# Optimization experiments

Measured on AMD Instinct MI355X. Metric: run time of the kernel, lower is better.

Reference implementation:

```python
import jax, jax.numpy as jnp
import numpy as np

N_EMBD = 512
N_HEAD = 8


def setup_inputs() -> dict:
    key = jax.random.key(0)
    k_x, k_aw, k_ab, k_pw, k_pb = jax.random.split(key, 5)
    B, T, E = 4, 2048, N_EMBD
    s = 1.0 / np.sqrt(E)
    return {
        "x": jax.random.normal(k_x, (B, T, E), dtype=jnp.float32),
        # torch Linear weight is [out, in]; store transposed for x @ W
        "c_attn_w": jax.random.uniform(k_aw, (E, 3 * E), jnp.float32, -s, s),
        "c_attn_b": jax.random.uniform(k_ab, (3 * E,), jnp.float32, -s, s),
        "c_proj_w": jax.random.uniform(k_pw, (E, E), jnp.float32, -s, s),
        "c_proj_b": jax.random.uniform(k_pb, (E,), jnp.float32, -s, s),
    }


def reference(x, c_attn_w, c_attn_b, c_proj_w, c_proj_b):
    B, T, E = x.shape
    H = N_HEAD
    D = E // H
    qkv = x @ c_attn_w + c_attn_b                      # [B,T,3E]
    q, k, v = jnp.split(qkv, 3, axis=2)
    # [B,T,E] -> [B,H,T,D]
    q = q.reshape(B, T, H, D).transpose(0, 2, 1, 3)
    k = k.reshape(B, T, H, D).transpose(0, 2, 1, 3)
    v = v.reshape(B, T, H, D).transpose(0, 2, 1, 3)
    scale = 1.0 / np.sqrt(D).astype(np.float32)
    scores = jnp.einsum("bhqd,bhkd->bhqk", q, k) * scale
    causal = jnp.tril(jnp.ones((T, T), dtype=bool))    # [T,T]
    scores = jnp.where(causal, scores, -jnp.inf)
    attn = jax.nn.softmax(scores, axis=-1)             # [B,H,T,T]
    y = jnp.einsum("bhqk,bhkd->bhqd", attn, v)         # [B,H,T,D]
    y = y.transpose(0, 2, 1, 3).reshape(B, T, E)
    return y @ c_proj_w + c_proj_b
```

## Files before the change

### kernel.cpp

```cpp
#include <hip/hip_runtime.h>
#include <math.h>

#define N_EMBD 512
#define N_HEAD 8
#define SEQ_T  2048
#define BATCH  4
#define QK_LD  1024

typedef __attribute__((ext_vector_type(8))) short bf16x8;
typedef __attribute__((ext_vector_type(4))) float f32x4;

#define CL 0.18033688f

#define WAITVM(N) asm volatile("s_waitcnt vmcnt(" #N ")" ::: "memory")

__device__ __forceinline__ unsigned short f2bf(float f) {
    union { float f; unsigned int u; } x; x.f = f;
    return (unsigned short)((x.u + 0x7FFFu + ((x.u >> 16) & 1u)) >> 16);
}
__device__ __forceinline__ unsigned pack_trunc(float a, float b) {
    union { float f; unsigned u; } x, y; x.f = a; y.f = b;
    return __builtin_amdgcn_perm(y.u, x.u, 0x07060302u);
}
__device__ __forceinline__ bf16x8 scale_frag(bf16x8 v, float c) {
    bf16x8 r;
    #pragma unroll
    for (int i = 0; i < 8; ++i) {
        union { unsigned u; float f; } x;
        x.u = ((unsigned)(unsigned short)v[i]) << 16;
        r[i] = (short)f2bf(x.f * c);
    }
    return r;
}

__device__ __forceinline__ void gl_lds16(const void* g, void* s) {
    __builtin_amdgcn_global_load_lds(
        (const __attribute__((address_space(1))) void*)g,
        (__attribute__((address_space(3))) void*)s, 16, 0, 0);
}

__global__ __launch_bounds__(256) void prep(
    const float* __restrict__ w1, unsigned short* __restrict__ w1t,
    const float* __restrict__ w2, unsigned short* __restrict__ w2t)
{
    __shared__ float t[32][33];
    const int bx = blockIdx.x, tid = threadIdx.x;
    const float* W; unsigned short* Wt; int N, tt, nb;
    if (bx < 768) { tt = bx;       W = w1; Wt = w1t; N = 1536; nb = 48; }
    else          { tt = bx - 768; W = w2; Wt = w2t; N = 512;  nb = 16; }
    const int n0 = (tt % nb) * 32, k0 = (tt / nb) * 32;
    const int tx = tid & 31, ty = tid >> 5;
    #pragma unroll
    for (int i = 0; i < 4; ++i)
        t[ty + i * 8][tx] = W[(size_t)(k0 + ty + i * 8) * N + n0 + tx];
    __syncthreads();
    #pragma unroll
    for (int i = 0; i < 4; ++i)
        Wt[(size_t)(n0 + ty + i * 8) * 512 + k0 + tx] = f2bf(t[tx][ty + i * 8]);
}

template <int BM, int BN, bool CVT_A, int OMODE>
__global__ __launch_bounds__(256) void gemm_mfma(
    const void* __restrict__ Asrc,
    const unsigned short* __restrict__ Bt,
    const float* __restrict__ bias,
    void* __restrict__ C, unsigned short* __restrict__ Cv,
    int N, int K, int xcdRows)
{
    constexpr int WMT = BM / 32, WNT = BN / 32;
    constexpr int SA = BM * 8 / 256, SB = BN * 8 / 256;
    __shared__ unsigned short SM[BM * 64 + BN * 64];
    unsigned short* As = SM;
    unsigned short* Bs = SM + BM * 64;

    const int tid  = threadIdx.x;
    const int wave = tid >> 6, lane = tid & 63;
    const int low  = lane & 15, quad = lane >> 4;
    const int wm   = (wave & 1) * (BM / 2), wn = (wave >> 1) * (BN / 2);

    const int xcd    = blockIdx.x & 7;
    const int within = blockIdx.x >> 3;
    const int rowBlk = xcd * xcdRows + (within % xcdRows);
    const int colBlk = within / xcdRows;
    const int row0 = rowBlk * BM, col0 = colBlk * BN;

    size_t a_src[SA]; int a_dst[SA];
    #pragma unroll
    for (int s = 0; s < SA; ++s) {
        const int p = tid + 256 * s;
        const int m = p >> 3, q = p & 7;
        a_src[s] = (size_t)(row0 + m) * K + q * 8;
        a_dst[s] = m * 64 + (q ^ (m & 7)) * 8;
    }
    size_t b_src[SB]; int b_dst[SB];
    #pragma unroll
    for (int s = 0; s < SB; ++s) {
        const int p = tid + 256 * s;
        const int m = p >> 3, q = p & 7;
        b_src[s] = (size_t)(col0 + m) * K + q * 8;
        b_dst[s] = m * 64 + (q ^ (m & 7)) * 8;
    }

    f32x4 acc[WMT][WNT];
    #pragma unroll
    for (int i = 0; i < WMT; ++i)
        #pragma unroll
        for (int j = 0; j < WNT; ++j) acc[i][j] = (f32x4){0.f, 0.f, 0.f, 0.f};

    bf16x8 ar[SA], br[SB];
    const float*          af32 = (const float*)Asrc;
    const unsigned short* a16  = (const unsigned short*)Asrc;

    #pragma unroll
    for (int s = 0; s < SA; ++s) {
        if (CVT_A) {
            const float4 f0 = *(const float4*)(af32 + a_src[s]);
            const float4 f1 = *(const float4*)(af32 + a_src[s] + 4);
            union { uint4 v; bf16x8 h; } u;
            u.v.x = pack_trunc(f0.x, f0.y); u.v.y = pack_trunc(f0.z, f0.w);
            u.v.z = pack_trunc(f1.x, f1.y); u.v.w = pack_trunc(f1.z, f1.w);
            ar[s] = u.h;
        } else {
            ar[s] = *(const bf16x8*)(a16 + a_src[s]);
        }
    }
    #pragma unroll
    for (int s = 0; s < SB; ++s) br[s] = *(const bf16x8*)(Bt + b_src[s]);

    const int NIT = K >> 6;
    for (int it = 0; it < NIT; ++it) {
        __syncthreads();
        #pragma unroll
        for (int s = 0; s < SA; ++s) *(bf16x8*)&As[a_dst[s]] = ar[s];
        #pragma unroll
        for (int s = 0; s < SB; ++s) *(bf16x8*)&Bs[b_dst[s]] = br[s];
        __syncthreads();

        if (it + 1 < NIT) {
            const int ko = (it + 1) * 64;
            #pragma unroll
            for (int s = 0; s < SA; ++s) {
                if (CVT_A) {
                    const float4 f0 = *(const float4*)(af32 + a_src[s] + ko);
                    const float4 f1 = *(const float4*)(af32 + a_src[s] + ko + 4);
                    union { uint4 v; bf16x8 h; } u;
                    u.v.x = pack_trunc(f0.x, f0.y); u.v.y = pack_trunc(f0.z, f0.w);
                    u.v.z = pack_trunc(f1.x, f1.y); u.v.w = pack_trunc(f1.z, f1.w);
                    ar[s] = u.h;
                } else {
                    ar[s] = *(const bf16x8*)(a16 + a_src[s] + ko);
                }
            }
            #pragma unroll
            for (int s = 0; s < SB; ++s) br[s] = *(const bf16x8*)(Bt + b_src[s] + ko);
        }

        #pragma unroll
        for (int h = 0; h < 2; ++h) {
            bf16x8 af[WMT], bfr[WNT];
            #pragma unroll
            for (int t = 0; t < WMT; ++t)
                af[t] = *(const bf16x8*)
                    &As[(wm + t * 16 + low) * 64 + (((h * 4 + quad) ^ (low & 7)) * 8)];
            #pragma unroll
            for (int t = 0; t < WNT; ++t)
                bfr[t] = *(const bf16x8*)
                    &Bs[(wn + t * 16 + low) * 64 + (((h * 4 + quad) ^ (low & 7)) * 8)];
            #pragma unroll
            for (int i = 0; i < WMT; ++i)
                #pragma unroll
                for (int j = 0; j < WNT; ++j)
                    acc[i][j] = __builtin_amdgcn_mfma_f32_16x16x32_bf16(
                        af[i], bfr[j], acc[i][j], 0, 0, 0);
        }
    }

    float bv[WNT];
    #pragma unroll
    for (int j = 0; j < WNT; ++j) bv[j] = bias[col0 + wn + j * 16 + low];

    const bool isV = (OMODE == 2) && (col0 >= 1024);
    if (isV) {
        unsigned short (*Cs)[130] = (unsigned short (*)[130])SM;
        const int bI = row0 >> 11;
        const int t0 = row0 & 2047;
        const int dloc = tid >> 2, sub = tid & 3;
        __syncthreads();
        #pragma unroll
        for (int p = 0; p < 2; ++p) {
            if ((wave >> 1) == p) {
                #pragma unroll
                for (int i = 0; i < WMT; ++i)
                    #pragma unroll
                    for (int j = 0; j < WNT; ++j)
                        #pragma unroll
                        for (int r = 0; r < 4; ++r)
                            Cs[j * 16 + low][wm + i * 16 + quad * 4 + r] =
                                f2bf(acc[i][j][r] + bv[j]);
            }
            __syncthreads();
            const int dglob = col0 - 1024 + p * 64 + dloc;
            unsigned short* vb =
                Cv + (((size_t)(bI * 512 + dglob)) << 11) + t0 + sub * 8;
            #pragma unroll
            for (int e = 0; e < 4; ++e)
                *(bf16x8*)(vb + e * 32) = *(const bf16x8*)&Cs[dloc][e * 32 + sub * 8];
            __syncthreads();
        }
    } else {
        #pragma unroll
        for (int i = 0; i < WMT; ++i)
            #pragma unroll
            for (int r = 0; r < 4; ++r) {
                const int row = row0 + wm + i * 16 + quad * 4 + r;
                #pragma unroll
                for (int j = 0; j < WNT; ++j) {
                    const int col = col0 + wn + j * 16 + low;
                    const float v = acc[i][j][r] + bv[j];
                    if (OMODE == 0)
                        ((float*)C)[(size_t)row * N + col] = v;
                    else if (OMODE == 1)
                        ((unsigned short*)C)[(size_t)row * N + col] = f2bf(v);
                    else
                        ((unsigned short*)C)[(size_t)row * QK_LD + col] = f2bf(v);
                }
            }
    }
}

template<bool MASK>
__device__ __forceinline__ void qk_step(
    const bf16x8 k00, const bf16x8 k01, const bf16x8 k10, const bf16x8 k11,
    const bf16x8 (&qf)[2][2], bf16x8 (&pf)[2], float (&lp)[2],
    const int qrel0, const int koffb)
{
    #pragma unroll
    for (int qb = 0; qb < 2; ++qb) {
        f32x4 s0 = (f32x4){0.f, 0.f, 0.f, 0.f};
        f32x4 s1 = (f32x4){0.f, 0.f, 0.f, 0.f};
        s0 = __builtin_amdgcn_mfma_f32_16x16x32_bf16(k00, qf[qb][0], s0, 0, 0, 0);
        s0 = __builtin_amdgcn_mfma_f32_16x16x32_bf16(k01, qf[qb][1], s0, 0, 0, 0);
        s1 = __builtin_amdgcn_mfma_f32_16x16x32_bf16(k10, qf[qb][0], s1, 0, 0, 0);
        s1 = __builtin_amdgcn_mfma_f32_16x16x32_bf16(k11, qf[qb][1], s1, 0, 0, 0);
        float p[8];
        #pragma unroll
        for (int r = 0; r < 4; ++r) {
            float v0 = s0[r], v1 = s1[r];
            if (MASK) {
                const int qrel = qrel0 + qb * 16;
                if (koffb + r     > qrel) v0 = -1e30f;
                if (koffb + r + 4 > qrel) v1 = -1e30f;
            }
            p[r]     = __builtin_amdgcn_exp2f(v0);
            p[r + 4] = __builtin_amdgcn_exp2f(v1);
        }
        #pragma unroll
        for (int e = 0; e < 8; ++e) {
            union { float f; unsigned u; } c; c.f = p[e];
            c.u &= 0xFFFF0000u; p[e] = c.f;
        }
        lp[qb] += ((p[0] + p[1]) + (p[2] + p[3])) + ((p[4] + p[5]) + (p[6] + p[7]));
        union { uint4 v; bf16x8 h; } u;
        u.v.x = pack_trunc(p[0], p[1]); u.v.y = pack_trunc(p[2], p[3]);
        u.v.z = pack_trunc(p[4], p[5]); u.v.w = pack_trunc(p[6], p[7]);
        pf[qb] = u.h;
    }
}

__global__ __launch_bounds__(256, 2) void attn_mfma(
    const unsigned short* __restrict__ qk,
    const unsigned short* __restrict__ vT,
    unsigned short* __restrict__ y)
{
    const int bh  = blockIdx.x & 31;
    const int pa  = blockIdx.x >> 5;
    const int b   = bh >> 3, h = bh & 7;
    const int qA0 = pa * 64;
    const int qB0 = (31 - pa) * 64;
    const int nA  = pa + 1, nB = 32 - pa;
    const int tid = threadIdx.x;
    const int wave = tid >> 6, lane = tid & 63;
    const int low  = lane & 15, quad = lane >> 4;
    const int kh   = wave & 1, qh = wave >> 1;

    __shared__ char smem[49152];
    unsigned short* KsB = (unsigned short*)smem;
    unsigned short* VsB = (unsigned short*)smem + 12288;

    const size_t base = (size_t)b * SEQ_T * QK_LD + h * 64;
    const unsigned short* qp = qk + base;
    const unsigned short* kp = qk + base + 512;
    const unsigned short* vp = vT + ((size_t)(b * 512 + h * 64) << 11);

    bf16x8 qf[2][2][2];
    #pragma unroll
    for (int s = 0; s < 2; ++s) {
        const int q0 = (s ? qB0 : qA0) + qh * 32;
        #pragma unroll
        for (int qb = 0; qb < 2; ++qb) {
            const size_t qr = (size_t)(q0 + qb * 16 + low) * QK_LD;
            #pragma unroll
            for (int dh = 0; dh < 2; ++dh)
                qf[s][qb][dh] = scale_frag(
                    *(const bf16x8*)(qp + qr + dh * 32 + quad * 8), CL);
        }
    }
    WAITVM(0);

    const int r8 = lane >> 3, s8 = lane & 7;
    const unsigned short* ksrc[2]; const unsigned short* vsrc[2]; int dst[2];
    #pragma unroll
    for (int ii = 0; ii < 2; ++ii) {
        const int hs = (r8 & 3) | (ii << 2);
        ksrc[ii] = kp + (size_t)(wave * 16 + ii * 8 + r8) * QK_LD + (s8 ^ hs) * 8;
        vsrc[ii] = vp + ((size_t)(wave * 16 + ii * 8 + r8) << 11) + (s8 ^ hs) * 8;
        dst[ii]  = (wave * 16 + ii * 8) * 64;
    }

    const int hkv = (low & 3) | (((low >> 2) & 1) << 2);
    const int hvv = (low & 3) | ((low >> 3) << 2);
    const int krow0 = kh * 32 + ((low >> 2) << 3) + (low & 3);
    const int koffK[2][2] = {
        { krow0 * 64 + ((quad    ) ^ hkv) * 8, krow0 * 64 + ((quad + 4) ^ hkv) * 8 },
        { (krow0+4)*64 + ((quad  ) ^ hkv) * 8, (krow0+4)*64 + ((quad + 4) ^ hkv) * 8 } };
    int voff[4];
    #pragma unroll
    for (int t = 0; t < 4; ++t)
        voff[t] = (t * 16 + low) * 64 + ((kh * 4 + quad) ^ hvv) * 8;
    const int koffb = kh * 32 + quad * 8;

    #pragma unroll
    for (int ii = 0; ii < 2; ++ii) {
        gl_lds16(ksrc[ii], KsB + dst[ii]);
        gl_lds16(vsrc[ii], VsB + dst[ii]);
    }
    #pragma unroll
    for (int ii = 0; ii < 2; ++ii) {
        gl_lds16(ksrc[ii] + (size_t)64 * QK_LD, KsB + 4096 + dst[ii]);
        gl_lds16(vsrc[ii] + 64,                 VsB + 4096 + dst[ii]);
    }

    f32x4 o[2][2][4];
    #pragma unroll
    for (int s = 0; s < 2; ++s)
        #pragma unroll
        for (int qb = 0; qb < 2; ++qb)
            #pragma unroll
            for (int t = 0; t < 4; ++t) o[s][qb][t] = (f32x4){0.f, 0.f, 0.f, 0.f};
    float lp[2][2] = {{0.f, 0.f}, {0.f, 0.f}};

    int cur = 0;
    for (int kc = 0; kc < nB; ++kc) {
        if (kc + 2 < nB) {
            const int sb = (cur == 0) ? 2 : cur - 1;
            const size_t kadv = (size_t)(kc + 2) * 64 * QK_LD;
            const int    vadv = (kc + 2) * 64;
            #pragma unroll
            for (int ii = 0; ii < 2; ++ii) {
                gl_lds16(ksrc[ii] + kadv, KsB + sb * 4096 + dst[ii]);
                gl_lds16(vsrc[ii] + vadv, VsB + sb * 4096 + dst[ii]);
            }
            WAITVM(8);
        } else if (kc + 1 < nB) {
            WAITVM(4);
        } else {
            WAITVM(0);
        }
        __builtin_amdgcn_s_barrier();
        __builtin_amdgcn_sched_barrier(0);

        const unsigned short* Kc = KsB + cur * 4096;
        const unsigned short* Vc = VsB + cur * 4096;
        bf16x8 kf[2][2], vf[4];
        #pragma unroll
        for (int kt = 0; kt < 2; ++kt)
            #pragma unroll
            for (int dh = 0; dh < 2; ++dh)
                kf[kt][dh] = *(const bf16x8*)&Kc[koffK[kt][dh]];
        #pragma unroll
        for (int t = 0; t < 4; ++t)
            vf[t] = *(const bf16x8*)&Vc[voff[t]];

        const int kc64 = kc * 64;
        bf16x8 pA[2], pB[2];
        const bool doA = (kc < nA);
        if (doA) {
            const int qrelA = qA0 + qh * 32 + low - kc64;
            if (kc == nA - 1)
                qk_step<true >(kf[0][0], kf[0][1], kf[1][0], kf[1][1], qf[0], pA, lp[0], qrelA, koffb);
            else
                qk_step<false>(kf[0][0], kf[0][1], kf[1][0], kf[1][1], qf[0], pA, lp[0], qrelA, koffb);
        }
        {
            const int qrelB = qB0 + qh * 32 + low - kc64;
            if (kc == nB - 1)
                qk_step<true >(kf[0][0], kf[0][1], kf[1][0], kf[1][1], qf[1], pB, lp[1], qrelB, koffb);
            else
                qk_step<false>(kf[0][0], kf[0][1], kf[1][0], kf[1][1], qf[1], pB, lp[1], qrelB, koffb);
        }

        if (doA) {
            #pragma unroll
            for (int t = 0; t < 4; ++t) {
                o[0][0][t] = __builtin_amdgcn_mfma_f32_16x16x32_bf16(pA[0], vf[t], o[0][0][t], 0, 0, 0);
                o[0][1][t] = __builtin_amdgcn_mfma_f32_16x16x32_bf16(pA[1], vf[t], o[0][1][t], 0, 0, 0);
            }
        }
        #pragma unroll
        for (int t = 0; t < 4; ++t) {
            o[1][0][t] = __builtin_amdgcn_mfma_f32_16x16x32_bf16(pB[0], vf[t], o[1][0][t], 0, 0, 0);
            o[1][1][t] = __builtin_amdgcn_mfma_f32_16x16x32_bf16(pB[1], vf[t], o[1][1][t], 0, 0, 0);
        }

        __builtin_amdgcn_s_barrier();
        cur = (cur == 2) ? 0 : cur + 1;
    }

    float* oB = (float*)smem;
    float* lB = (float*)(smem + 33792);

    #pragma unroll
    for (int s = 0; s < 2; ++s)
        #pragma unroll
        for (int qb = 0; qb < 2; ++qb) {
            float v = lp[s][qb];
            v += __shfl_xor(v, 16);
            v += __shfl_xor(v, 32);
            if (quad == 0) lB[(kh * 2 + qh) * 64 + (s * 2 + qb) * 16 + low] = v;
        }
    if (kh == 1) {
        #pragma unroll
        for (int s = 0; s < 2; ++s)
            #pragma unroll
            for (int qb = 0; qb < 2; ++qb)
                #pragma unroll
                for (int t = 0; t < 4; ++t)
                    #pragma unroll
                    for (int r = 0; r < 4; ++r)
                        oB[qh * 4224 + ((s * 2 + qb) * 16 + quad * 4 + r) * 66
                           + low + t * 16] = o[s][qb][t][r];
    }
    __syncthreads();
    if (kh == 0) {
        #pragma unroll
        for (int s = 0; s < 2; ++s) {
            const int q0 = (s ? qB0 : qA0) + qh * 32;
            #pragma unroll
            for (int qb = 0; qb < 2; ++qb) {
                #pragma unroll
                for (int r = 0; r < 4; ++r) {
                    const int ri = (s * 2 + qb) * 16 + quad * 4 + r;
                    const float l = lB[qh * 64 + ri] + lB[128 + qh * 64 + ri];
                    const float rl = 1.f / l;
                    const int qrow = q0 + qb * 16 + quad * 4 + r;
                    unsigned short* yp =
                        y + (size_t)(b * SEQ_T + qrow) * N_EMBD + h * 64 + low;
                    #pragma unroll
                    for (int t = 0; t < 4; ++t)
                        yp[t * 16] = f2bf(
                            (o[s][qb][t][r] + oB[qh * 4224 + ri * 66 + low + t * 16]) * rl);
                }
            }
        }
    }
}

extern "C" void kernel_launch(void* const* d_in, const int* in_sizes, int n_in,
                              void* d_out, int out_size, void* d_ws, size_t ws_size,
                              hipStream_t stream)
{
    const float* x      = (const float*)d_in[0];
    const float* attn_w = (const float*)d_in[1];
    const float* attn_b = (const float*)d_in[2];
    const float* proj_w = (const float*)d_in[3];
    const float* proj_b = (const float*)d_in[4];
    float*       out    = (float*)d_out;

    char* ws = (char*)d_ws;
    unsigned short* qk_bf = (unsigned short*)(ws);
    unsigned short* vT    = (unsigned short*)(ws + 16777216);
    unsigned short* y_bf  = (unsigned short*)(ws + 25165824);
    unsigned short* w1t   = (unsigned short*)(ws + 33554432);
    unsigned short* w2t   = (unsigned short*)(ws + 35127296);

    prep<<<1024, 256, 0, stream>>>(attn_w, w1t, proj_w, w2t);

    gemm_mfma<128, 128, true, 2><<<dim3(768), 256, 0, stream>>>(
        x, w1t, attn_b, qk_bf, vT, 1536, N_EMBD, 8);

    attn_mfma<<<dim3(512), 256, 0, stream>>>(qk_bf, vT, y_bf);

    gemm_mfma<64, 128, false, 0><<<dim3(512), 256, 0, stream>>>(
        y_bf, w2t, proj_b, out, nullptr, N_EMBD, N_EMBD, 16);
}
```

Before: 137.1 us.

## Process 128-key tiles with double buffering and MFMA-based row-sum accumulation

Doubles the key tile per iteration from 64 to 128 rows, switching from a triple-buffered 64-key ring to a double-buffered 128-key scheme in 64KB LDS with a new V swizzle. Softmax row sums are now computed by MFMA against a vector of bf16 ones instead of VALU truncation and adds, and the wave-level shuffle reduction at the end is dropped. s_setprio is raised around the MFMA section. The aim is fewer barriers and loop iterations and less VALU work, at the cost of more LDS per block (which may reduce occupancy) and coarser causal masking on the diagonal tile.

New measurement: 150.1 us. 1.1x slower.

```diff
diff --git a/kernel.cpp b/kernel.cpp
--- a/kernel.cpp
+++ b/kernel.cpp
@@ -229,9 +229,9 @@
 }
 
 template<bool MASK>
-__device__ __forceinline__ void qk_step(
+__device__ __forceinline__ void qk_slice(
     const bf16x8 k00, const bf16x8 k01, const bf16x8 k10, const bf16x8 k11,
-    const bf16x8 (&qf)[2][2], bf16x8 (&pf)[2], float (&lp)[2],
+    const bf16x8 (&qf)[2][2], bf16x8 (&pf)[2],
     const int qrel0, const int koffb)
 {
     #pragma unroll
@@ -254,12 +254,6 @@
             p[r]     = __builtin_amdgcn_exp2f(v0);
             p[r + 4] = __builtin_amdgcn_exp2f(v1);
         }
-        #pragma unroll
-        for (int e = 0; e < 8; ++e) {
-            union { float f; unsigned u; } c; c.f = p[e];
-            c.u &= 0xFFFF0000u; p[e] = c.f;
-        }
-        lp[qb] += ((p[0] + p[1]) + (p[2] + p[3])) + ((p[4] + p[5]) + (p[6] + p[7]));
         union { uint4 v; bf16x8 h; } u;
         u.v.x = pack_trunc(p[0], p[1]); u.v.y = pack_trunc(p[2], p[3]);
         u.v.z = pack_trunc(p[4], p[5]); u.v.w = pack_trunc(p[6], p[7]);
@@ -277,15 +271,16 @@
     const int b   = bh >> 3, h = bh & 7;
     const int qA0 = pa * 64;
     const int qB0 = (31 - pa) * 64;
-    const int nA  = pa + 1, nB = 32 - pa;
+    const int nTA = (pa >> 1) + 1;
+    const int nT  = (33 - pa) >> 1;
     const int tid = threadIdx.x;
     const int wave = tid >> 6, lane = tid & 63;
     const int low  = lane & 15, quad = lane >> 4;
     const int kh   = wave & 1, qh = wave >> 1;
 
-    __shared__ char smem[49152];
+    __shared__ char smem[65536];
     unsigned short* KsB = (unsigned short*)smem;
-    unsigned short* VsB = (unsigned short*)smem + 12288;
+    unsigned short* VsB = (unsigned short*)(smem + 32768);
 
     const size_t base = (size_t)b * SEQ_T * QK_LD + h * 64;
     const unsigned short* qp = qk + base;
@@ -308,37 +303,48 @@
     WAITVM(0);
 
     const int r8 = lane >> 3, s8 = lane & 7;
-    const unsigned short* ksrc[2]; const unsigned short* vsrc[2]; int dst[2];
-    #pragma unroll
-    for (int ii = 0; ii < 2; ++ii) {
-        const int hs = (r8 & 3) | (ii << 2);
-        ksrc[ii] = kp + (size_t)(wave * 16 + ii * 8 + r8) * QK_LD + (s8 ^ hs) * 8;
-        vsrc[ii] = vp + ((size_t)(wave * 16 + ii * 8 + r8) << 11) + (s8 ^ hs) * 8;
-        dst[ii]  = (wave * 16 + ii * 8) * 64;
+    const int r4 = lane >> 4, s16 = lane & 15;
+    const unsigned short* ksrc[4]; int kdst[4];
+    const unsigned short* vsrc[4]; int vdst[4];
+    #pragma unroll
+    for (int ii = 0; ii < 4; ++ii) {
+        const int krow = wave * 32 + ii * 8 + r8;
+        const int khash = (r8 & 3) | ((ii & 1) << 2);
+        ksrc[ii] = kp + (size_t)krow * QK_LD + (s8 ^ khash) * 8;
+        kdst[ii] = (wave * 32 + ii * 8) * 64;
+        const int vrow = wave * 16 + ii * 4 + r4;
+        vsrc[ii] = vp + ((size_t)vrow << 11) + (s16 ^ (vrow & 15)) * 8;
+        vdst[ii] = (wave * 16 + ii * 4) * 128;
     }
 
     const int hkv = (low & 3) | (((low >> 2) & 1) << 2);
-    const int hvv = (low & 3) | ((low >> 3) << 2);
-    const int krow0 = kh * 32 + ((low >> 2) << 3) + (low & 3);
-    const int koffK[2][2] = {
-        { krow0 * 64 + ((quad    ) ^ hkv) * 8, krow0 * 64 + ((quad + 4) ^ hkv) * 8 },
-        { (krow0+4)*64 + ((quad  ) ^ hkv) * 8, (krow0+4)*64 + ((quad + 4) ^ hkv) * 8 } };
-    int voff[4];
-    #pragma unroll
-    for (int t = 0; t < 4; ++t)
-        voff[t] = (t * 16 + low) * 64 + ((kh * 4 + quad) ^ hvv) * 8;
-    const int koffb = kh * 32 + quad * 8;
-
-    #pragma unroll
-    for (int ii = 0; ii < 2; ++ii) {
-        gl_lds16(ksrc[ii], KsB + dst[ii]);
-        gl_lds16(vsrc[ii], VsB + dst[ii]);
-    }
-    #pragma unroll
-    for (int ii = 0; ii < 2; ++ii) {
-        gl_lds16(ksrc[ii] + (size_t)64 * QK_LD, KsB + 4096 + dst[ii]);
-        gl_lds16(vsrc[ii] + 64,                 VsB + 4096 + dst[ii]);
-    }
+    const int rowperm = ((low >> 2) << 3) + (low & 3);
+    int koffK[2][2][2];
+    #pragma unroll
+    for (int ks = 0; ks < 2; ++ks)
+        #pragma unroll
+        for (int kt = 0; kt < 2; ++kt)
+            #pragma unroll
+            for (int dh = 0; dh < 2; ++dh)
+                koffK[ks][kt][dh] = (kh * 64 + ks * 32 + rowperm + kt * 4) * 64
+                                  + ((quad + 4 * dh) ^ hkv) * 8;
+    int voff[2][4];
+    #pragma unroll
+    for (int ks = 0; ks < 2; ++ks)
+        #pragma unroll
+        for (int t = 0; t < 4; ++t)
+            voff[ks][t] = (t * 16 + low) * 128
+                        + ((kh * 8 + ks * 4 + quad) ^ low) * 8;
+    const int kofs0 = kh * 64 + quad * 8;
+
+    #pragma unroll
+    for (int ii = 0; ii < 4; ++ii) gl_lds16(ksrc[ii], KsB + kdst[ii]);
+    #pragma unroll
+    for (int ii = 0; ii < 4; ++ii) gl_lds16(vsrc[ii], VsB + vdst[ii]);
+
+    bf16x8 ones;
+    #pragma unroll
+    for (int i = 0; i < 8; ++i) ones[i] = (short)0x3F80;
 
     f32x4 o[2][2][4];
     #pragma unroll
@@ -347,73 +353,111 @@
         for (int qb = 0; qb < 2; ++qb)
             #pragma unroll
             for (int t = 0; t < 4; ++t) o[s][qb][t] = (f32x4){0.f, 0.f, 0.f, 0.f};
-    float lp[2][2] = {{0.f, 0.f}, {0.f, 0.f}};
+    f32x4 lacc[2][2];
+    #pragma unroll
+    for (int s = 0; s < 2; ++s)
+        #pragma unroll
+        for (int qb = 0; qb < 2; ++qb) lacc[s][qb] = (f32x4){0.f, 0.f, 0.f, 0.f};
 
     int cur = 0;
-    for (int kc = 0; kc < nB; ++kc) {
-        if (kc + 2 < nB) {
-            const int sb = (cur == 0) ? 2 : cur - 1;
-            const size_t kadv = (size_t)(kc + 2) * 64 * QK_LD;
-            const int    vadv = (kc + 2) * 64;
-            #pragma unroll
-            for (int ii = 0; ii < 2; ++ii) {
-                gl_lds16(ksrc[ii] + kadv, KsB + sb * 4096 + dst[ii]);
-                gl_lds16(vsrc[ii] + vadv, VsB + sb * 4096 + dst[ii]);
-            }
+    for (int kc = 0; kc < nT; ++kc) {
+        if (kc + 1 < nT) {
+            const size_t kadv = (size_t)(kc + 1) * 128 * QK_LD;
+            const int    vadv = (kc + 1) * 128;
+            const int    bo   = (cur ^ 1) * 8192;
+            #pragma unroll
+            for (int ii = 0; ii < 4; ++ii)
+                gl_lds16(ksrc[ii] + kadv, KsB + bo + kdst[ii]);
+            #pragma unroll
+            for (int ii = 0; ii < 4; ++ii)
+                gl_lds16(vsrc[ii] + vadv, VsB + bo + vdst[ii]);
             WAITVM(8);
-        } else if (kc + 1 < nB) {
-            WAITVM(4);
         } else {
             WAITVM(0);
         }
         __builtin_amdgcn_s_barrier();
         __builtin_amdgcn_sched_barrier(0);
 
-        const unsigned short* Kc = KsB + cur * 4096;
-        const unsigned short* Vc = VsB + cur * 4096;
-        bf16x8 kf[2][2], vf[4];
-        #pragma unroll
-        for (int kt = 0; kt < 2; ++kt)
-            #pragma unroll
-            for (int dh = 0; dh < 2; ++dh)
-                kf[kt][dh] = *(const bf16x8*)&Kc[koffK[kt][dh]];
-        #pragma unroll
-        for (int t = 0; t < 4; ++t)
-            vf[t] = *(const bf16x8*)&Vc[voff[t]];
-
-        const int kc64 = kc * 64;
-        bf16x8 pA[2], pB[2];
-        const bool doA = (kc < nA);
+        const unsigned short* Kc = KsB + cur * 8192;
+        const unsigned short* Vc = VsB + cur * 8192;
+        bf16x8 kf[2][2][2], vfr[2][4];
+        #pragma unroll
+        for (int ks = 0; ks < 2; ++ks)
+            #pragma unroll
+            for (int kt = 0; kt < 2; ++kt)
+                #pragma unroll
+                for (int dh = 0; dh < 2; ++dh)
+                    kf[ks][kt][dh] = *(const bf16x8*)&Kc[koffK[ks][kt][dh]];
+        #pragma unroll
+        for (int ks = 0; ks < 2; ++ks)
+            #pragma unroll
+            for (int t = 0; t < 4; ++t)
+                vfr[ks][t] = *(const bf16x8*)&Vc[voff[ks][t]];
+
+        const int kb0 = kc * 128;
+        bf16x8 pA0[2], pA1[2], pB0[2], pB1[2];
+        const bool doA = (kc < nTA);
+
+        __builtin_amdgcn_s_setprio(1);
         if (doA) {
-            const int qrelA = qA0 + qh * 32 + low - kc64;
-            if (kc == nA - 1)
-                qk_step<true >(kf[0][0], kf[0][1], kf[1][0], kf[1][1], qf[0], pA, lp[0], qrelA, koffb);
-            else
-                qk_step<false>(kf[0][0], kf[0][1], kf[1][0], kf[1][1], qf[0], pA, lp[0], qrelA, koffb);
+            const int qrelA = qA0 + qh * 32 + low - kb0;
+            if (kc == nTA - 1) {
+                qk_slice<true >(kf[0][0][0], kf[0][0][1], kf[0][1][0], kf[0][1][1],
+                                qf[0], pA0, qrelA, kofs0);
+                qk_slice<true >(kf[1][0][0], kf[1][0][1], kf[1][1][0], kf[1][1][1],
+                                qf[0], pA1, qrelA, kofs0 + 32);
+            } else {
+                qk_slice<false>(kf[0][0][0], kf[0][0][1], kf[0][1][0], kf[0][1][1],
+                                qf[0], pA0, qrelA, kofs0);
+                qk_slice<false>(kf[1][0][0], kf[1][0][1], kf[1][1][0], kf[1][1][1],
+                                qf[0], pA1, qrelA, kofs0 + 32);
+            }
         }
         {
-            const int qrelB = qB0 + qh * 32 + low - kc64;
-            if (kc == nB - 1)
-                qk_step<true >(kf[0][0], kf[0][1], kf[1][0], kf[1][1], qf[1], pB, lp[1], qrelB, koffb);
-            else
-                qk_step<false>(kf[0][0], kf[0][1], kf[1][0], kf[1][1], qf[1], pB, lp[1], qrelB, koffb);
+            const int qrelB = qB0 + qh * 32 + low - kb0;
+            if (kc == nT - 1) {
+                qk_slice<true >(kf[0][0][0], kf[0][0][1], kf[0][1][0], kf[0][1][1],
+                                qf[1], pB0, qrelB, kofs0);
+                qk_slice<true >(kf[1][0][0], kf[1][0][1], kf[1][1][0], kf[1][1][1],
+                                qf[1], pB1, qrelB, kofs0 + 32);
+            } else {
+                qk_slice<false>(kf[0][0][0], kf[0][0][1], kf[0][1][0], kf[0][1][1],
+                                qf[1], pB0, qrelB, kofs0);
+                qk_slice<false>(kf[1][0][0], kf[1][0][1], kf[1][1][0], kf[1][1][1],
+                                qf[1], pB1, qrelB, kofs0 + 32);
+            }
         }
 
         if (doA) {
             #pragma unroll
+            for (int qb = 0; qb < 2; ++qb) {
+                lacc[0][qb] = __builtin_amdgcn_mfma_f32_16x16x32_bf16(pA0[qb], ones, lacc[0][qb], 0, 0, 0);
+                lacc[0][qb] = __builtin_amdgcn_mfma_f32_16x16x32_bf16(pA1[qb], ones, lacc[0][qb], 0, 0, 0);
+            }
+            #pragma unroll
             for (int t = 0; t < 4; ++t) {
-                o[0][0][t] = __builtin_amdgcn_mfma_f32_16x16x32_bf16(pA[0], vf[t], o[0][0][t], 0, 0, 0);
-                o[0][1][t] = __builtin_amdgcn_mfma_f32_16x16x32_bf16(pA[1], vf[t], o[0][1][t], 0, 0, 0);
-            }
+                o[0][0][t] = __builtin_amdgcn_mfma_f32_16x16x32_bf16(pA0[0], vfr[0][t], o[0][0][t], 0, 0, 0);
+                o[0][0][t] = __builtin_amdgcn_mfma_f32_16x16x32_bf16(pA1[0], vfr[1][t], o[0][0][t], 0, 0, 0);
+                o[0][1][t] = __builtin_amdgcn_mfma_f32_16x16x32_bf16(pA0[1], vfr[0][t], o[0][1][t], 0, 0, 0);
+                o[0][1][t] = __builtin_amdgcn_mfma_f32_16x16x32_bf16(pA1[1], vfr[1][t], o[0][1][t], 0, 0, 0);
+            }
+        }
+        #pragma unroll
+        for (int qb = 0; qb < 2; ++qb) {
+            lacc[1][qb] = __builtin_amdgcn_mfma_f32_16x16x32_bf16(pB0[qb], ones, lacc[1][qb], 0, 0, 0);
+            lacc[1][qb] = __builtin_amdgcn_mfma_f32_16x16x32_bf16(pB1[qb], ones, lacc[1][qb], 0, 0, 0);
         }
         #pragma unroll
         for (int t = 0; t < 4; ++t) {
-            o[1][0][t] = __builtin_amdgcn_mfma_f32_16x16x32_bf16(pB[0], vf[t], o[1][0][t], 0, 0, 0);
-            o[1][1][t] = __builtin_amdgcn_mfma_f32_16x16x32_bf16(pB[1], vf[t], o[1][1][t], 0, 0, 0);
-        }
+            o[1][0][t] = __builtin_amdgcn_mfma_f32_16x16x32_bf16(pB0[0], vfr[0][t], o[1][0][t], 0, 0, 0);
+            o[1][0][t] = __builtin_amdgcn_mfma_f32_16x16x32_bf16(pB1[0], vfr[1][t], o[1][0][t], 0, 0, 0);
+            o[1][1][t] = __builtin_amdgcn_mfma_f32_16x16x32_bf16(pB0[1], vfr[0][t], o[1][1][t], 0, 0, 0);
+            o[1][1][t] = __builtin_amdgcn_mfma_f32_16x16x32_bf16(pB1[1], vfr[1][t], o[1][1][t], 0, 0, 0);
+        }
+        __builtin_amdgcn_s_setprio(0);
 
         __builtin_amdgcn_s_barrier();
-        cur = (cur == 2) ? 0 : cur + 1;
+        cur ^= 1;
     }
 
     float* oB = (float*)smem;
@@ -422,12 +466,13 @@
     #pragma unroll
     for (int s = 0; s < 2; ++s)
         #pragma unroll
-        for (int qb = 0; qb < 2; ++qb) {
-            float v = lp[s][qb];
-            v += __shfl_xor(v, 16);
-            v += __shfl_xor(v, 32);
-            if (quad == 0) lB[(kh * 2 + qh) * 64 + (s * 2 + qb) * 16 + low] = v;
-        }
+        for (int qb = 0; qb < 2; ++qb)
+            if (low == 0) {
+                #pragma unroll
+                for (int r = 0; r < 4; ++r)
+                    lB[(kh * 2 + qh) * 64 + (s * 2 + qb) * 16 + quad * 4 + r]
+                        = lacc[s][qb][r];
+            }
     if (kh == 1) {
         #pragma unroll
         for (int s = 0; s < 2; ++s)
```
